# Optimization experiments

Hardware: AMD Instinct MI355X
Metric: run time of the kernel (lower is better)

## Reference

```python
import jax, jax.numpy as jnp
import numpy as np

N_HEADS, D_MODEL, D_HEAD = 16, 1024, 64
LN_EPS = 1e-5


def setup_inputs() -> dict:
    key = jax.random.key(0)
    ks = jax.random.split(key, 12)
    bs, s = 2, 2048
    hd = N_HEADS * D_HEAD
    sc = 0.02
    return {
        "q": jax.random.normal(ks[0], (bs, s, D_MODEL), jnp.float32),
        "kv": jax.random.normal(ks[1], (bs, s, D_MODEL), jnp.float32),
        "Wq": jax.random.normal(ks[2], (D_MODEL, hd), jnp.float32) * sc,
        "bq": jnp.zeros((hd,), jnp.float32),
        "Wk": jax.random.normal(ks[3], (D_MODEL, hd), jnp.float32) * sc,
        "bk": jnp.zeros((hd,), jnp.float32),
        "Wv": jax.random.normal(ks[4], (D_MODEL, hd), jnp.float32) * sc,
        "bv": jnp.zeros((hd,), jnp.float32),
        "Wo": jax.random.normal(ks[5], (hd, D_MODEL), jnp.float32) * sc,
        "bo": jnp.zeros((D_MODEL,), jnp.float32),
        "gamma": jnp.ones((D_MODEL,), jnp.float32),
        "beta": jnp.zeros((D_MODEL,), jnp.float32),
    }


def _split_heads(x):
    # [b, s, H*D] -> [b, H, s, D]
    b, s, _ = x.shape
    return x.reshape(b, s, N_HEADS, D_HEAD).transpose(0, 2, 1, 3)


def reference(q, kv, Wq, bq, Wk, bk, Wv, bv, Wo, bo, gamma, beta):
    wq = _split_heads(q @ Wq + bq)   # [b,H,Sq,D]
    wk = _split_heads(kv @ Wk + bk)  # [b,H,Sk,D]
    wv = _split_heads(kv @ Wv + bv)  # [b,H,Sk,D]
    scores = jnp.einsum("bhqd,bhkd->bhqk", wq, wk) / jnp.sqrt(
        jnp.asarray(D_HEAD, wq.dtype)
    )
    probs = jax.nn.softmax(scores, axis=-1)  # dropout p=0 -> identity
    attn = jnp.einsum("bhqk,bhkd->bhqd", probs, wv)
    b, _, sq, _ = attn.shape
    attn = attn.transpose(0, 2, 1, 3).reshape(b, sq, N_HEADS * D_HEAD)
    res = q + (attn @ Wo + bo)
    # LayerNorm over last dim
    mu = jnp.mean(res, axis=-1, keepdims=True)
    var = jnp.var(res, axis=-1, keepdims=True)
    return (res - mu) * jax.lax.rsqrt(var + LN_EPS) * gamma + beta
```

## Files before the change

kernel.cpp:

```cpp
#include <hip/hip_runtime.h>
#include <hip/hip_bf16.h>


#define DM 1024
#define SEQ 2048
#define NB 2
#define NH 16
#define DH 64

typedef __attribute__((ext_vector_type(8))) short bf16x8;
typedef __attribute__((ext_vector_type(4))) float f32x4;
typedef __attribute__((ext_vector_type(4))) unsigned int u32x4;

__device__ __forceinline__ float bf2f(short s) {
  unsigned u = ((unsigned)(unsigned short)s) << 16;
  return __builtin_bit_cast(float, u);
}
__device__ __forceinline__ short f2bf(float f) {
  unsigned u = __builtin_bit_cast(unsigned, f);
  u += 0x7fffu + ((u >> 16) & 1u);
  return (short)(u >> 16);
}
__device__ __forceinline__ unsigned cvt_pk_bf16(float lo, float hi) {
  unsigned r;
  asm("v_cvt_pk_bf16_f32 %0, %1, %2" : "=v"(r) : "v"(lo), "v"(hi));
  return r;
}
__device__ __forceinline__ float exp2_fast(float x) {
  float r;
  asm("v_exp_f32 %0, %1" : "=v"(r) : "v"(x));
  return r;
}

#define GLL16(gsrc, ldst)                                                     \
  __builtin_amdgcn_global_load_lds(                                           \
      (const __attribute__((address_space(1))) void*)(gsrc),                  \
      (__attribute__((address_space(3))) void*)(ldst), 16, 0, 0)

#define WAIT_VM(N)                                                            \
  asm volatile("s_waitcnt vmcnt(" #N ")" ::: "memory");                       \
  __builtin_amdgcn_s_barrier();                                               \
  __builtin_amdgcn_sched_barrier(0)

__global__ __launch_bounds__(256) void k_transpose(
    const float* __restrict__ Wq, const float* __restrict__ Wk,
    const float* __restrict__ Wv, const float* __restrict__ Wo,
    short* __restrict__ Wt_all) {
  const int z = blockIdx.z;
  const float* src = (z == 0) ? Wq : (z == 1) ? Wk : (z == 2) ? Wv : Wo;
  short* dst = Wt_all + (size_t)z * (DM * DM);
  __shared__ float t[32][33];
  const int n0 = blockIdx.x * 32, k0 = blockIdx.y * 32;
  const int tx = threadIdx.x, ty = threadIdx.y;
#pragma unroll
  for (int i = 0; i < 32; i += 8)
    t[ty + i][tx] = src[(size_t)(k0 + ty + i) * DM + n0 + tx];
  __syncthreads();
#pragma unroll
  for (int i = 0; i < 32; i += 8)
    dst[(size_t)(n0 + ty + i) * DM + k0 + tx] = f2bf(t[tx][ty + i]);
}

__global__ __launch_bounds__(256) void k_cvt(const float* __restrict__ q,
                                             const float* __restrict__ kv,
                                             short* __restrict__ qb,
                                             short* __restrict__ kvb) {
  const int i = blockIdx.x * 256 + threadIdx.x;
  const int half = 524288;
  const float* src = (i < half) ? q : kv;
  short* dst = (i < half) ? qb : kvb;
  const size_t j = (size_t)((i < half) ? i : i - half) * 8;
  const float4 a = *(const float4*)(src + j);
  const float4 b = *(const float4*)(src + j + 4);
  u32x4 pw;
  pw[0] = cvt_pk_bf16(a.x, a.y);
  pw[1] = cvt_pk_bf16(a.z, a.w);
  pw[2] = cvt_pk_bf16(b.x, b.y);
  pw[3] = cvt_pk_bf16(b.z, b.w);
  *(bf16x8*)(dst + j) = __builtin_bit_cast(bf16x8, pw);
}

__device__ __forceinline__ void gemm_body64(short* As, short* Bs,
                                            const short* __restrict__ X,
                                            const short* __restrict__ Wt,
                                            const float* __restrict__ bias,
                                            short* __restrict__ out,
                                            int vt_mode, float cscale,
                                            int bx, int by) {
  const int tid = threadIdx.x;
  const int w = tid >> 6, l = tid & 63;
  const int g = l >> 4, qi = l & 15;
  const int n0 = bx * 128;
  const int m0 = by * 128;
  const int wr = w >> 1, wc = w & 1;

  f32x4 acc[4][4];
#pragma unroll
  for (int m = 0; m < 4; m++)
#pragma unroll
    for (int n = 0; n < 4; n++) acc[m][n] = (f32x4){0.f, 0.f, 0.f, 0.f};

  const int srow = w * 8 + (l >> 3);
  const int scol = ((l & 7) ^ ((l >> 3) & 7)) * 8;
  const short* Ag = X + (size_t)(m0 + srow) * DM + scol;
  const short* Bg = Wt + (size_t)(n0 + srow) * DM + scol;

  for (int k0 = 0; k0 < DM; k0 += 64) {
    __syncthreads();
#pragma unroll
    for (int j = 0; j < 4; j++) {
      GLL16(Ag + (size_t)(j * 32) * DM + k0, As + j * 2048 + w * 512);
      GLL16(Bg + (size_t)(j * 32) * DM + k0, Bs + j * 2048 + w * 512);
    }
    __syncthreads();

#pragma unroll
    for (int kk = 0; kk < 2; kk++) {
      bf16x8 a[4], b[4];
#pragma unroll
      for (int m = 0; m < 4; m++)
        a[m] = *(const bf16x8*)&As[(wr * 64 + m * 16 + qi) * 64 +
                                   (((kk * 4 + g) ^ (qi & 7)) * 8)];
#pragma unroll
      for (int n = 0; n < 4; n++)
        b[n] = *(const bf16x8*)&Bs[(wc * 64 + n * 16 + qi) * 64 +
                                   (((kk * 4 + g) ^ (qi & 7)) * 8)];
#pragma unroll
      for (int m = 0; m < 4; m++)
#pragma unroll
        for (int n = 0; n < 4; n++)
          acc[m][n] = __builtin_amdgcn_mfma_f32_16x16x32_bf16(a[m], b[n],
                                                              acc[m][n], 0, 0, 0);
    }
  }

  const int col0 = n0 + wc * 64;
  const int row0 = m0 + wr * 64;
  float bfv[4];
#pragma unroll
  for (int n = 0; n < 4; n++) bfv[n] = bias[col0 + n * 16 + qi];

  if (!vt_mode) {
#pragma unroll
    for (int m = 0; m < 4; m++) {
#pragma unroll
      for (int n = 0; n < 4; n++) {
        const int col = col0 + n * 16 + qi;
#pragma unroll
        for (int r = 0; r < 4; r++) {
          const int row = row0 + m * 16 + g * 4 + r;
          out[(size_t)row * DM + col] = f2bf((acc[m][n][r] + bfv[n]) * cscale);
        }
      }
    }
  } else {
#pragma unroll
    for (int m = 0; m < 4; m++) {
      const int s_base = row0 + m * 16 + g * 4;
      const int bb = s_base >> 11;
      const int s = s_base & (SEQ - 1);
#pragma unroll
      for (int n = 0; n < 4; n++) {
        const int col = col0 + n * 16 + qi;
        const int h = col >> 6, d = col & 63;
        ushort4 v;
        v.x = (unsigned short)f2bf(acc[m][n][0] + bfv[n]);
        v.y = (unsigned short)f2bf(acc[m][n][1] + bfv[n]);
        v.z = (unsigned short)f2bf(acc[m][n][2] + bfv[n]);
        v.w = (unsigned short)f2bf(acc[m][n][3] + bfv[n]);
        *(ushort4*)&out[(((size_t)bb * NH + h) * DH + d) * SEQ + s] = v;
      }
    }
  }
}

__device__ __forceinline__ void xcd_remap(int& bx, int& by) {
  const int lin2 = blockIdx.x + 8 * blockIdx.y;
  const int xcd = lin2 & 7, jj = lin2 >> 3;
  bx = jj & 7;
  by = xcd * 4 + (jj >> 3);
}

__global__ __launch_bounds__(256) void k_gemm_qkv(
    const short* __restrict__ qb, const short* __restrict__ kvb,
    const short* __restrict__ Wt, const float* __restrict__ bq,
    const float* __restrict__ bk, const float* __restrict__ bv,
    short* __restrict__ qm, short* __restrict__ km, short* __restrict__ vtb) {
  __shared__ short As[8192], Bs[8192];
  const int z = blockIdx.z;
  const short* X = (z == 0) ? qb : kvb;
  const short* W = Wt + (size_t)z * (DM * DM);
  const float* bias = (z == 0) ? bq : (z == 1) ? bk : bv;
  short* out = (z == 0) ? qm : (z == 1) ? km : vtb;
  const float cs = (z == 0) ? 0.18033688011112042f : 1.0f;
  int bx, by;
  xcd_remap(bx, by);
  gemm_body64(As, Bs, X, W, bias, out, z == 2, cs, bx, by);
}

__global__ __launch_bounds__(256) void k_gemm_o(
    const short* __restrict__ attn, const short* __restrict__ Wto,
    const float* __restrict__ bo, short* __restrict__ om) {
  __shared__ short As[8192], Bs[8192];
  int bx, by;
  xcd_remap(bx, by);
  gemm_body64(As, Bs, attn, Wto, bo, om, 0, 1.0f, bx, by);
}

__global__ __launch_bounds__(512) void k_attn(const short* __restrict__ qm,
                                              const short* __restrict__ km,
                                              const short* __restrict__ vt,
                                              short* __restrict__ attn) {
  __shared__ short lds[3][8192];

  const int lin = blockIdx.x;
  const int x = lin & 7, j = lin >> 3;
  const int pair = x + 8 * (j >> 3), qb = j & 7;
  const int h = pair & 15, bb = pair >> 4;
  const int q0 = qb * 256;

  const int tid = threadIdx.x;
  const int w = tid >> 6, l = tid & 63;
  const int g = l >> 4, qi = l & 15;

  const size_t bbS = (size_t)bb * SEQ;
  const size_t vbase = ((size_t)(bb * NH + h)) * DH * SEQ;
  const short* __restrict__ kmh = km + bbS * DM + h * DH;

  const int skey = tid >> 3;
  const int sslot = tid & 7;
  const int kgq = sslot ^ ((skey >> 1) & 7);
  const int vkb = sslot ^ (skey & 7);
  const short* __restrict__ srcK0 = kmh + (size_t)skey * DM + kgq * 8;
  const short* __restrict__ srcV0 = vt + vbase + (size_t)skey * SEQ + vkb * 8;

#define STAGE(buf, kk0)                                                       \
  {                                                                           \
    GLL16(srcK0 + (size_t)(kk0)*DM, &lds[buf][w * 512]);                      \
    GLL16(srcV0 + (kk0), &lds[buf][4096 + w * 512]);                          \
  }

  const int rowA = q0 + w * 32 + qi;
  const short* QpA = qm + (bbS + rowA) * DM + h * DH;
  const bf16x8 qA0 = *(const bf16x8*)(QpA + 8 * g);
  const bf16x8 qA1 = *(const bf16x8*)(QpA + 32 + 8 * g);
  const bf16x8 qB0 = *(const bf16x8*)(QpA + 16 * DM + 8 * g);
  const bf16x8 qB1 = *(const bf16x8*)(QpA + 16 * DM + 32 + 8 * g);

  float ssA[4], ssB[4];
#pragma unroll
  for (int i = 0; i < 4; i++) { ssA[i] = 0.f; ssB[i] = 0.f; }
  f32x4 oA[4], oB[4];
#pragma unroll
  for (int f = 0; f < 4; f++) {
    oA[f] = (f32x4){0.f, 0.f, 0.f, 0.f};
    oB[f] = (f32x4){0.f, 0.f, 0.f, 0.f};
  }

  const int xA = (g ^ (qi & 7)) * 8;
  const int xB = ((4 + g) ^ (qi & 7)) * 8;

  auto tile = [&](const short* Ks, const short* Vs) {
#pragma unroll
    for (int s = 0; s < 2; s++) {
      const int r0 = (32 * s + 2 * qi) * 64;
      const bf16x8 k00 = *(const bf16x8*)&Ks[r0 + xA];
      const bf16x8 k01 = *(const bf16x8*)&Ks[r0 + xB];
      const bf16x8 k10 = *(const bf16x8*)&Ks[r0 + 64 + xA];
      const bf16x8 k11 = *(const bf16x8*)&Ks[r0 + 64 + xB];

      f32x4 sA0 = (f32x4){0.f, 0.f, 0.f, 0.f};
      f32x4 sA1 = (f32x4){0.f, 0.f, 0.f, 0.f};
      f32x4 sB0 = (f32x4){0.f, 0.f, 0.f, 0.f};
      f32x4 sB1 = (f32x4){0.f, 0.f, 0.f, 0.f};
      __builtin_amdgcn_s_setprio(1);
      sA0 = __builtin_amdgcn_mfma_f32_16x16x32_bf16(k00, qA0, sA0, 0, 0, 0);
      sA0 = __builtin_amdgcn_mfma_f32_16x16x32_bf16(k01, qA1, sA0, 0, 0, 0);
      sA1 = __builtin_amdgcn_mfma_f32_16x16x32_bf16(k10, qA0, sA1, 0, 0, 0);
      sA1 = __builtin_amdgcn_mfma_f32_16x16x32_bf16(k11, qA1, sA1, 0, 0, 0);
      sB0 = __builtin_amdgcn_mfma_f32_16x16x32_bf16(k00, qB0, sB0, 0, 0, 0);
      sB0 = __builtin_amdgcn_mfma_f32_16x16x32_bf16(k01, qB1, sB0, 0, 0, 0);
      sB1 = __builtin_amdgcn_mfma_f32_16x16x32_bf16(k10, qB0, sB1, 0, 0, 0);
      sB1 = __builtin_amdgcn_mfma_f32_16x16x32_bf16(k11, qB1, sB1, 0, 0, 0);
      __builtin_amdgcn_s_setprio(0);

      float eA0[4], eA1[4], eB0[4], eB1[4];
#pragma unroll
      for (int r = 0; r < 4; r++) {
        eA0[r] = exp2_fast(sA0[r]);
        eA1[r] = exp2_fast(sA1[r]);
        eB0[r] = exp2_fast(sB0[r]);
        eB1[r] = exp2_fast(sB1[r]);
      }
#pragma unroll
      for (int r = 0; r < 4; r++) {
        ssA[r] += eA0[r] + eA1[r];
        ssB[r] += eB0[r] + eB1[r];
      }
      u32x4 pwA, pwB;
#pragma unroll
      for (int r = 0; r < 4; r++) {
        pwA[r] = cvt_pk_bf16(eA0[r], eA1[r]);
        pwB[r] = cvt_pk_bf16(eB0[r], eB1[r]);
      }
      const bf16x8 pbA = __builtin_bit_cast(bf16x8, pwA);
      const bf16x8 pbB = __builtin_bit_cast(bf16x8, pwB);

      const int vx = ((4 * s + g) ^ (qi & 7)) * 8;
      __builtin_amdgcn_s_setprio(1);
#pragma unroll
      for (int f = 0; f < 4; f++) {
        const bf16x8 vv = *(const bf16x8*)&Vs[(qi + 16 * f) * 64 + vx];
        oA[f] = __builtin_amdgcn_mfma_f32_16x16x32_bf16(vv, pbA, oA[f], 0, 0, 0);
        oB[f] = __builtin_amdgcn_mfma_f32_16x16x32_bf16(vv, pbB, oB[f], 0, 0, 0);
      }
      __builtin_amdgcn_s_setprio(0);
    }
  };

  STAGE(0, 0);
  STAGE(1, 64);
  int cur = 0;
  for (int t = 0; t < 31; ++t) {
    WAIT_VM(2);
    if (t < 30) {
      int n2 = cur + 2;
      if (n2 >= 3) n2 -= 3;
      STAGE(n2, (t + 2) * 64);
    }
    tile(&lds[cur][0], &lds[cur][4096]);
    cur = (cur + 1 == 3) ? 0 : cur + 1;
  }
  WAIT_VM(0);
  tile(&lds[cur][0], &lds[cur][4096]);

  float sa = (ssA[0] + ssA[1]) + (ssA[2] + ssA[3]);
  sa += __shfl_xor(sa, 16);
  sa += __shfl_xor(sa, 32);
  const float invA = 1.f / sa;
  float sb = (ssB[0] + ssB[1]) + (ssB[2] + ssB[3]);
  sb += __shfl_xor(sb, 16);
  sb += __shfl_xor(sb, 32);
  const float invB = 1.f / sb;

  short* OpA = attn + (bbS + rowA) * DM + h * DH;
#pragma unroll
  for (int f = 0; f < 4; f++) {
    ushort4 v;
    v.x = (unsigned short)f2bf(oA[f][0] * invA);
    v.y = (unsigned short)f2bf(oA[f][1] * invA);
    v.z = (unsigned short)f2bf(oA[f][2] * invA);
    v.w = (unsigned short)f2bf(oA[f][3] * invA);
    *(ushort4*)(OpA + f * 16 + g * 4) = v;
    ushort4 u;
    u.x = (unsigned short)f2bf(oB[f][0] * invB);
    u.y = (unsigned short)f2bf(oB[f][1] * invB);
    u.z = (unsigned short)f2bf(oB[f][2] * invB);
    u.w = (unsigned short)f2bf(oB[f][3] * invB);
    *(ushort4*)(OpA + 16 * DM + f * 16 + g * 4) = u;
  }
#undef STAGE
}

__global__ __launch_bounds__(256) void k_ln(const float* __restrict__ q,
                                            const short* __restrict__ om,
                                            const float* __restrict__ gamma,
                                            const float* __restrict__ beta,
                                            float* __restrict__ out) {
  const int row = blockIdx.x;
  const int t = threadIdx.x;
  const int w = t >> 6, l = t & 63;
  const size_t base = (size_t)row * DM + t * 4;
  const float4 qv = *(const float4*)(q + base);
  const ushort4 ov = *(const ushort4*)(om + base);
  float v[4];
  v[0] = qv.x + bf2f((short)ov.x);
  v[1] = qv.y + bf2f((short)ov.y);
  v[2] = qv.z + bf2f((short)ov.z);
  v[3] = qv.w + bf2f((short)ov.w);
  float s = v[0] + v[1] + v[2] + v[3];
  float s2 = v[0] * v[0] + v[1] * v[1] + v[2] * v[2] + v[3] * v[3];
#pragma unroll
  for (int off = 32; off >= 1; off >>= 1) {
    s += __shfl_xor(s, off);
    s2 += __shfl_xor(s2, off);
  }
  __shared__ float ps[4], ps2[4];
  if (l == 0) {
    ps[w] = s;
    ps2[w] = s2;
  }
  __syncthreads();
  const float St = ps[0] + ps[1] + ps[2] + ps[3];
  const float S2t = ps2[0] + ps2[1] + ps2[2] + ps2[3];
  const float mu = St * (1.f / 1024.f);
  float var = S2t * (1.f / 1024.f) - mu * mu;
  const float rstd = rsqrtf(var + 1e-5f);
  const float4 gv = *(const float4*)(gamma + t * 4);
  const float4 bv = *(const float4*)(beta + t * 4);
  float4 ovv;
  ovv.x = (v[0] - mu) * rstd * gv.x + bv.x;
  ovv.y = (v[1] - mu) * rstd * gv.y + bv.y;
  ovv.z = (v[2] - mu) * rstd * gv.z + bv.z;
  ovv.w = (v[3] - mu) * rstd * gv.w + bv.w;
  *(float4*)(out + base) = ovv;
}

extern "C" void kernel_launch(void* const* d_in, const int* in_sizes, int n_in,
                              void* d_out, int out_size, void* d_ws, size_t ws_size,
                              hipStream_t stream) {
  const float* q = (const float*)d_in[0];
  const float* kv = (const float*)d_in[1];
  const float* Wq = (const float*)d_in[2];
  const float* bq = (const float*)d_in[3];
  const float* Wk = (const float*)d_in[4];
  const float* bk = (const float*)d_in[5];
  const float* Wv = (const float*)d_in[6];
  const float* bv = (const float*)d_in[7];
  const float* Wo = (const float*)d_in[8];
  const float* bo = (const float*)d_in[9];
  const float* gamma = (const float*)d_in[10];
  const float* beta = (const float*)d_in[11];

  short* ws = (short*)d_ws;
  short* Wt = ws;
  short* qb16 = ws + 4u * 1048576u;
  short* kvb16 = qb16 + 4194304u;
  short* qm = kvb16 + 4194304u;
  short* km = qm + 4194304u;
  short* vtb = km + 4194304u;
  short* attnb = qb16;
  short* om = kvb16;

  hipLaunchKernelGGL(k_transpose, dim3(32, 32, 4), dim3(32, 8), 0, stream,
                     Wq, Wk, Wv, Wo, Wt);
  hipLaunchKernelGGL(k_cvt, dim3(4096), dim3(256), 0, stream, q, kv, qb16, kvb16);
  hipLaunchKernelGGL(k_gemm_qkv, dim3(8, 32, 3), dim3(256), 0, stream,
                     qb16, kvb16, Wt, bq, bk, bv, qm, km, vtb);
  hipLaunchKernelGGL(k_attn, dim3(256), dim3(512), 0, stream,
                     qm, km, vtb, attnb);
  hipLaunchKernelGGL(k_gemm_o, dim3(8, 32, 1), dim3(256), 0, stream,
                     attnb, Wt + 3u * 1048576u, bo, om);
  hipLaunchKernelGGL(k_ln, dim3(4096), dim3(256), 0, stream,
                     q, om, gamma, beta, (float*)d_out);
}
```

Before: 121.8 us.

## Split attention keys across two blocks with combine pass; double-buffer GEMM K-loop

The attention kernel now splits each (batch, head, query-block) over two key halves. This doubles the grid to 512 blocks so there are more blocks than CUs. Each half writes unnormalized bf16 partial outputs and row sums, and a new k_combine kernel adds them and normalizes. Separately, the projection GEMMs move from a single-buffered BK=64 loop with two barriers to a double-buffered BK=32 loop with prefetch and one barrier per step. The cost is an extra kernel launch, extra global traffic for the partials, and an added bf16 rounding of the partial outputs.

New measurement: 136.0 us. 1.12x slower.

```diff
diff --git a/kernel.cpp b/kernel.cpp
--- a/kernel.cpp
+++ b/kernel.cpp
@@ -80,7 +80,7 @@
   *(bf16x8*)(dst + j) = __builtin_bit_cast(bf16x8, pw);
 }
 
-__device__ __forceinline__ void gemm_body64(short* As, short* Bs,
+__device__ __forceinline__ void gemm_body32(short (*As)[4096], short (*Bs)[4096],
                                             const short* __restrict__ X,
                                             const short* __restrict__ Wt,
                                             const float* __restrict__ bias,
@@ -100,38 +100,43 @@
 #pragma unroll
     for (int n = 0; n < 4; n++) acc[m][n] = (f32x4){0.f, 0.f, 0.f, 0.f};
 
-  const int srow = w * 8 + (l >> 3);
-  const int scol = ((l & 7) ^ ((l >> 3) & 7)) * 8;
+  const int srow = w * 16 + (l >> 2);
+  const int scol = ((l & 3) ^ ((l >> 2) & 3)) * 8;
   const short* Ag = X + (size_t)(m0 + srow) * DM + scol;
   const short* Bg = Wt + (size_t)(n0 + srow) * DM + scol;
 
-  for (int k0 = 0; k0 < DM; k0 += 64) {
+  auto stage = [&](int buf, int k0) {
+#pragma unroll
+    for (int jj = 0; jj < 2; ++jj) {
+      GLL16(Ag + (size_t)(jj * 64) * DM + k0, &As[buf][jj * 2048 + w * 512]);
+      GLL16(Bg + (size_t)(jj * 64) * DM + k0, &Bs[buf][jj * 2048 + w * 512]);
+    }
+  };
+
+  auto compute = [&](int buf) {
+    bf16x8 a[4], b[4];
+    const int xo = (g ^ (qi & 3)) * 8;
+#pragma unroll
+    for (int m = 0; m < 4; m++)
+      a[m] = *(const bf16x8*)&As[buf][(wr * 64 + m * 16 + qi) * 32 + xo];
+#pragma unroll
+    for (int n = 0; n < 4; n++)
+      b[n] = *(const bf16x8*)&Bs[buf][(wc * 64 + n * 16 + qi) * 32 + xo];
+    __builtin_amdgcn_s_setprio(1);
+#pragma unroll
+    for (int m = 0; m < 4; m++)
+#pragma unroll
+      for (int n = 0; n < 4; n++)
+        acc[m][n] = __builtin_amdgcn_mfma_f32_16x16x32_bf16(a[m], b[n],
+                                                            acc[m][n], 0, 0, 0);
+    __builtin_amdgcn_s_setprio(0);
+  };
+
+  stage(0, 0);
+  for (int ks = 0; ks < 32; ++ks) {
     __syncthreads();
-#pragma unroll
-    for (int j = 0; j < 4; j++) {
-      GLL16(Ag + (size_t)(j * 32) * DM + k0, As + j * 2048 + w * 512);
-      GLL16(Bg + (size_t)(j * 32) * DM + k0, Bs + j * 2048 + w * 512);
-    }
-    __syncthreads();
-
-#pragma unroll
-    for (int kk = 0; kk < 2; kk++) {
-      bf16x8 a[4], b[4];
-#pragma unroll
-      for (int m = 0; m < 4; m++)
-        a[m] = *(const bf16x8*)&As[(wr * 64 + m * 16 + qi) * 64 +
-                                   (((kk * 4 + g) ^ (qi & 7)) * 8)];
-#pragma unroll
-      for (int n = 0; n < 4; n++)
-        b[n] = *(const bf16x8*)&Bs[(wc * 64 + n * 16 + qi) * 64 +
-                                   (((kk * 4 + g) ^ (qi & 7)) * 8)];
-#pragma unroll
-      for (int m = 0; m < 4; m++)
-#pragma unroll
-        for (int n = 0; n < 4; n++)
-          acc[m][n] = __builtin_amdgcn_mfma_f32_16x16x32_bf16(a[m], b[n],
-                                                              acc[m][n], 0, 0, 0);
-    }
+    if (ks < 31) stage((ks + 1) & 1, (ks + 1) * 32);
+    compute(ks & 1);
   }
 
   const int col0 = n0 + wc * 64;
@@ -186,7 +191,7 @@
     const short* __restrict__ Wt, const float* __restrict__ bq,
     const float* __restrict__ bk, const float* __restrict__ bv,
     short* __restrict__ qm, short* __restrict__ km, short* __restrict__ vtb) {
-  __shared__ short As[8192], Bs[8192];
+  __shared__ short As[2][4096], Bs[2][4096];
   const int z = blockIdx.z;
   const short* X = (z == 0) ? qb : kvb;
   const short* W = Wt + (size_t)z * (DM * DM);
@@ -195,29 +200,34 @@
   const float cs = (z == 0) ? 0.18033688011112042f : 1.0f;
   int bx, by;
   xcd_remap(bx, by);
-  gemm_body64(As, Bs, X, W, bias, out, z == 2, cs, bx, by);
+  gemm_body32(As, Bs, X, W, bias, out, z == 2, cs, bx, by);
 }
 
 __global__ __launch_bounds__(256) void k_gemm_o(
     const short* __restrict__ attn, const short* __restrict__ Wto,
     const float* __restrict__ bo, short* __restrict__ om) {
-  __shared__ short As[8192], Bs[8192];
+  __shared__ short As[2][4096], Bs[2][4096];
   int bx, by;
   xcd_remap(bx, by);
-  gemm_body64(As, Bs, attn, Wto, bo, om, 0, 1.0f, bx, by);
+  gemm_body32(As, Bs, attn, Wto, bo, om, 0, 1.0f, bx, by);
 }
 
 __global__ __launch_bounds__(512) void k_attn(const short* __restrict__ qm,
                                               const short* __restrict__ km,
                                               const short* __restrict__ vt,
-                                              short* __restrict__ attn) {
+                                              short* __restrict__ Op0,
+                                              short* __restrict__ Op1,
+                                              float* __restrict__ ssf) {
   __shared__ short lds[3][8192];
 
   const int lin = blockIdx.x;
-  const int x = lin & 7, j = lin >> 3;
-  const int pair = x + 8 * (j >> 3), qb = j & 7;
+  const int xcd = lin & 7, j = lin >> 3;
+  const int pair = xcd + 8 * (j >> 4);
+  const int sub = j & 15;
+  const int qb = sub >> 1, half = sub & 1;
   const int h = pair & 15, bb = pair >> 4;
   const int q0 = qb * 256;
+  const int keybase = half * 1024;
 
   const int tid = threadIdx.x;
   const int w = tid >> 6, l = tid & 63;
@@ -318,15 +328,15 @@
     }
   };
 
-  STAGE(0, 0);
-  STAGE(1, 64);
+  STAGE(0, keybase);
+  STAGE(1, keybase + 64);
   int cur = 0;
-  for (int t = 0; t < 31; ++t) {
+  for (int t = 0; t < 15; ++t) {
     WAIT_VM(2);
-    if (t < 30) {
+    if (t < 14) {
       int n2 = cur + 2;
       if (n2 >= 3) n2 -= 3;
-      STAGE(n2, (t + 2) * 64);
+      STAGE(n2, keybase + (t + 2) * 64);
     }
     tile(&lds[cur][0], &lds[cur][4096]);
     cur = (cur + 1 == 3) ? 0 : cur + 1;
@@ -334,32 +344,52 @@
   WAIT_VM(0);
   tile(&lds[cur][0], &lds[cur][4096]);
 
-  float sa = (ssA[0] + ssA[1]) + (ssA[2] + ssA[3]);
-  sa += __shfl_xor(sa, 16);
-  sa += __shfl_xor(sa, 32);
-  const float invA = 1.f / sa;
-  float sb = (ssB[0] + ssB[1]) + (ssB[2] + ssB[3]);
-  sb += __shfl_xor(sb, 16);
-  sb += __shfl_xor(sb, 32);
-  const float invB = 1.f / sb;
-
-  short* OpA = attn + (bbS + rowA) * DM + h * DH;
-#pragma unroll
-  for (int f = 0; f < 4; f++) {
-    ushort4 v;
-    v.x = (unsigned short)f2bf(oA[f][0] * invA);
-    v.y = (unsigned short)f2bf(oA[f][1] * invA);
-    v.z = (unsigned short)f2bf(oA[f][2] * invA);
-    v.w = (unsigned short)f2bf(oA[f][3] * invA);
-    *(ushort4*)(OpA + f * 16 + g * 4) = v;
-    ushort4 u;
-    u.x = (unsigned short)f2bf(oB[f][0] * invB);
-    u.y = (unsigned short)f2bf(oB[f][1] * invB);
-    u.z = (unsigned short)f2bf(oB[f][2] * invB);
-    u.w = (unsigned short)f2bf(oB[f][3] * invB);
-    *(ushort4*)(OpA + 16 * DM + f * 16 + g * 4) = u;
-  }
+  short* Opb = half ? Op1 : Op0;
+
+#define WRITE_P(SS, O, ROWOFF)                                                \
+  {                                                                           \
+    float ss_ = (SS[0] + SS[1]) + (SS[2] + SS[3]);                            \
+    ss_ += __shfl_xor(ss_, 16);                                               \
+    ss_ += __shfl_xor(ss_, 32);                                               \
+    if (g == 0)                                                               \
+      ssf[(size_t)(half * 16 + h) * 4096 + bb * SEQ + rowA + (ROWOFF)] = ss_; \
+    short* Op_ = Opb + (bbS + rowA + (ROWOFF)) * DM + h * DH;                 \
+    _Pragma("unroll") for (int f = 0; f < 4; f++) {                           \
+      ushort4 v_;                                                             \
+      v_.x = (unsigned short)f2bf(O[f][0]);                                   \
+      v_.y = (unsigned short)f2bf(O[f][1]);                                   \
+      v_.z = (unsigned short)f2bf(O[f][2]);                                   \
+      v_.w = (unsigned short)f2bf(O[f][3]);                                   \
+      *(ushort4*)(Op_ + f * 16 + g * 4) = v_;                                 \
+    }                                                                         \
+  }
+
+  WRITE_P(ssA, oA, 0)
+  WRITE_P(ssB, oB, 16)
 #undef STAGE
+#undef WRITE_P
+}
+
+__global__ __launch_bounds__(256) void k_combine(const short* __restrict__ Op0,
+                                                 const short* __restrict__ Op1,
+                                                 const float* __restrict__ ssf,
+                                                 short* __restrict__ out) {
+  const int row = blockIdx.x;
+  const int t = threadIdx.x;
+  const int col = t * 4;
+  const int h = col >> 6;
+  const float s0 = ssf[(size_t)h * 4096 + row];
+  const float s1 = ssf[(size_t)(16 + h) * 4096 + row];
+  const float inv = 1.f / (s0 + s1);
+  const size_t idx = (size_t)row * DM + col;
+  const ushort4 a = *(const ushort4*)(Op0 + idx);
+  const ushort4 b = *(const ushort4*)(Op1 + idx);
+  ushort4 o;
+  o.x = (unsigned short)f2bf((bf2f((short)a.x) + bf2f((short)b.x)) * inv);
+  o.y = (unsigned short)f2bf((bf2f((short)a.y) + bf2f((short)b.y)) * inv);
+  o.z = (unsigned short)f2bf((bf2f((short)a.z) + bf2f((short)b.z)) * inv);
+  o.w = (unsigned short)f2bf((bf2f((short)a.w) + bf2f((short)b.w)) * inv);
+  *(ushort4*)(out + idx) = o;
 }
 
 __global__ __launch_bounds__(256) void k_ln(const float* __restrict__ q,
@@ -429,7 +459,7 @@
   short* qm = kvb16 + 4194304u;
   short* km = qm + 4194304u;
   short* vtb = km + 4194304u;
-  short* attnb = qb16;
+  float* ssf = (float*)ws;
   short* om = kvb16;
 
   hipLaunchKernelGGL(k_transpose, dim3(32, 32, 4), dim3(32, 8), 0, stream,
@@ -437,10 +467,12 @@
   hipLaunchKernelGGL(k_cvt, dim3(4096), dim3(256), 0, stream, q, kv, qb16, kvb16);
   hipLaunchKernelGGL(k_gemm_qkv, dim3(8, 32, 3), dim3(256), 0, stream,
                      qb16, kvb16, Wt, bq, bk, bv, qm, km, vtb);
-  hipLaunchKernelGGL(k_attn, dim3(256), dim3(512), 0, stream,
-                     qm, km, vtb, attnb);
+  hipLaunchKernelGGL(k_attn, dim3(512), dim3(512), 0, stream,
+                     qm, km, vtb, qb16, kvb16, ssf);
+  hipLaunchKernelGGL(k_combine, dim3(4096), dim3(256), 0, stream,
+                     qb16, kvb16, ssf, qm);
   hipLaunchKernelGGL(k_gemm_o, dim3(8, 32, 1), dim3(256), 0, stream,
-                     attnb, Wt + 3u * 1048576u, bo, om);
+                     qm, Wt + 3u * 1048576u, bo, om);
   hipLaunchKernelGGL(k_ln, dim3(4096), dim3(256), 0, stream,
                      q, om, gamma, beta, (float*)d_out);
 }
```

## Load V directly from global into registers and double-buffer only K in LDS

Applied to the files above, without the earlier changes.

The attention kernel stops staging V tiles through LDS. Each wave now reads its V fragments straight from global memory into registers at the start of each tile. Only K goes through LDS, with a simple double buffer guarded by __syncthreads instead of the triple-buffered explicit vmcnt pipeline. This cuts LDS footprint and LDS read traffic, but every wave re-fetches the same V data from L2. The direct global loads also sit on the critical path with no prefetch, and they share the vmcnt counter with the K prefetch.

Result: slower. 165.1 us (+35.5%).

```diff
diff --git a/kernel.cpp b/kernel.cpp
--- a/kernel.cpp
+++ b/kernel.cpp
@@ -36,11 +36,6 @@
   __builtin_amdgcn_global_load_lds(                                           \
       (const __attribute__((address_space(1))) void*)(gsrc),                  \
       (__attribute__((address_space(3))) void*)(ldst), 16, 0, 0)
-
-#define WAIT_VM(N)                                                            \
-  asm volatile("s_waitcnt vmcnt(" #N ")" ::: "memory");                       \
-  __builtin_amdgcn_s_barrier();                                               \
-  __builtin_amdgcn_sched_barrier(0)
 
 __global__ __launch_bounds__(256) void k_transpose(
     const float* __restrict__ Wq, const float* __restrict__ Wk,
@@ -211,7 +206,7 @@
                                               const short* __restrict__ km,
                                               const short* __restrict__ vt,
                                               short* __restrict__ attn) {
-  __shared__ short lds[3][8192];
+  __shared__ short lds[2][4096];
 
   const int lin = blockIdx.x;
   const int x = lin & 7, j = lin >> 3;
@@ -230,15 +225,11 @@
   const int skey = tid >> 3;
   const int sslot = tid & 7;
   const int kgq = sslot ^ ((skey >> 1) & 7);
-  const int vkb = sslot ^ (skey & 7);
   const short* __restrict__ srcK0 = kmh + (size_t)skey * DM + kgq * 8;
-  const short* __restrict__ srcV0 = vt + vbase + (size_t)skey * SEQ + vkb * 8;
-
-#define STAGE(buf, kk0)                                                       \
-  {                                                                           \
-    GLL16(srcK0 + (size_t)(kk0)*DM, &lds[buf][w * 512]);                      \
-    GLL16(srcV0 + (kk0), &lds[buf][4096 + w * 512]);                          \
-  }
+
+#define STAGE(buf, kk0) GLL16(srcK0 + (size_t)(kk0)*DM, &lds[buf][w * 512])
+
+  const short* __restrict__ Vg = vt + vbase + (size_t)qi * SEQ + 8 * g;
 
   const int rowA = q0 + w * 32 + qi;
   const short* QpA = qm + (bbS + rowA) * DM + h * DH;
@@ -260,7 +251,13 @@
   const int xA = (g ^ (qi & 7)) * 8;
   const int xB = ((4 + g) ^ (qi & 7)) * 8;
 
-  auto tile = [&](const short* Ks, const short* Vs) {
+  auto tile = [&](const short* Ks, int kk0) {
+    bf16x8 vv0[4], vv1[4];
+#pragma unroll
+    for (int f = 0; f < 4; f++) {
+      vv0[f] = *(const bf16x8*)(Vg + (size_t)(16 * f) * SEQ + kk0);
+      vv1[f] = *(const bf16x8*)(Vg + (size_t)(16 * f) * SEQ + kk0 + 32);
+    }
 #pragma unroll
     for (int s = 0; s < 2; s++) {
       const int r0 = (32 * s + 2 * qi) * 64;
@@ -306,33 +303,23 @@
       const bf16x8 pbA = __builtin_bit_cast(bf16x8, pwA);
       const bf16x8 pbB = __builtin_bit_cast(bf16x8, pwB);
 
-      const int vx = ((4 * s + g) ^ (qi & 7)) * 8;
       __builtin_amdgcn_s_setprio(1);
 #pragma unroll
       for (int f = 0; f < 4; f++) {
-        const bf16x8 vv = *(const bf16x8*)&Vs[(qi + 16 * f) * 64 + vx];
-        oA[f] = __builtin_amdgcn_mfma_f32_16x16x32_bf16(vv, pbA, oA[f], 0, 0, 0);
-        oB[f] = __builtin_amdgcn_mfma_f32_16x16x32_bf16(vv, pbB, oB[f], 0, 0, 0);
+        const bf16x8 vf = s ? vv1[f] : vv0[f];
+        oA[f] = __builtin_amdgcn_mfma_f32_16x16x32_bf16(vf, pbA, oA[f], 0, 0, 0);
+        oB[f] = __builtin_amdgcn_mfma_f32_16x16x32_bf16(vf, pbB, oB[f], 0, 0, 0);
       }
       __builtin_amdgcn_s_setprio(0);
     }
   };
 
   STAGE(0, 0);
-  STAGE(1, 64);
-  int cur = 0;
-  for (int t = 0; t < 31; ++t) {
-    WAIT_VM(2);
-    if (t < 30) {
-      int n2 = cur + 2;
-      if (n2 >= 3) n2 -= 3;
-      STAGE(n2, (t + 2) * 64);
-    }
-    tile(&lds[cur][0], &lds[cur][4096]);
-    cur = (cur + 1 == 3) ? 0 : cur + 1;
-  }
-  WAIT_VM(0);
-  tile(&lds[cur][0], &lds[cur][4096]);
+  for (int t = 0; t < 32; ++t) {
+    __syncthreads();
+    if (t < 31) STAGE((t + 1) & 1, (t + 1) * 64);
+    tile(&lds[t & 1][0], t * 64);
+  }
 
   float sa = (ssA[0] + ssA[1]) + (ssA[2] + ssA[3]);
   sa += __shfl_xor(sa, 16);
```
